# Optimization experiments

Measured on AMD Instinct MI355X. Metric: run time of the kernel, lower is better.

## Reference

```python
import jax, jax.numpy as jnp
import numpy as np

NSITES = 262144
ZP1 = 13  # coordination number Z=12, plus the self row


def setup_inputs() -> dict:
    key = jax.random.key(0)
    k1, k2, k3, k4 = jax.random.split(key, 4)
    In = jax.random.normal(k1, (4, 8, NSITES), dtype=jnp.float32)
    NNsites = jax.random.randint(k2, (ZP1, NSITES), 0, NSITES, dtype=jnp.int32)
    Weights = jax.random.normal(k3, (8, 8, 16), dtype=jnp.float32)  # (K, C_out, 2*C_in)
    bias = jax.random.normal(k4, (8, 8), dtype=jnp.float32)         # (K, C_out)
    return {"In": In, "NNsites": NNsites, "Weights": Weights, "bias": bias}


def reference(In, NNsites, Weights, bias):
    # Original math per neighbor z:
    #   total = concat([In, In[:,:,NN[1+z]]], axis=1)            # (B, 2C_in, N)
    #   o[b,n,k,co] = sum_i W[k,co,i]*total[b,i,n] + bias[k,co]
    #   o summed over channels k, then softplus, accumulated over z.
    # Sum over k commutes with the linear map, so use effective weights.
    C_in = In.shape[1]
    Weff = Weights.sum(axis=0)          # (C_out, 2*C_in)
    beff = bias.sum(axis=0)             # (C_out,)
    Ws, Wn = Weff[:, :C_in], Weff[:, C_in:]
    # self contribution, identical for every z
    self_part = jnp.einsum('oi,bin->bon', Ws, In)          # (B, C_out, N)
    # gather all Z neighbor shells at once: (B, C_in, Z, N)
    neigh = In[:, :, NNsites[1:]]
    neigh_out = jnp.einsum('oi,bizn->bozn', Wn, neigh)     # (B, C_out, Z, N)
    pre = self_part[:, :, None, :] + neigh_out + beff[None, :, None, None]
    return jax.nn.softplus(pre).sum(axis=2)                # (B, C_out, N)
```

## Files before the change

### kernel.cpp

```cpp
#include <hip/hip_runtime.h>
#include <hip/hip_fp16.h>

#define NSITES 262144

struct alignas(16) H8 { __half2 h[4]; };
typedef __attribute__((ext_vector_type(2))) float floatx2;
typedef __attribute__((ext_vector_type(4))) unsigned int uintx4;


__global__ __launch_bounds__(256) void prep_kernel(
    const float* __restrict__ In,
    const float* __restrict__ Weights,
    const float* __restrict__ bias,
    uint2* __restrict__ G8,
    H8*    __restrict__ Sp)
{
    __shared__ float ws[8][8], wn[8][8], be[8];
    int t = threadIdx.x;
    if (t < 64) {
        int o = t >> 3, k = t & 7;
        float s0 = 0.f, s1 = 0.f;
        #pragma unroll
        for (int s = 0; s < 8; ++s) {
            s0 += Weights[s*128 + o*16 + k];
            s1 += Weights[s*128 + o*16 + 8 + k];
        }
        ws[o][k] = s0; wn[o][k] = s1;
    } else if (t < 72) {
        int o = t - 64;
        float s = 0.f;
        #pragma unroll
        for (int q = 0; q < 8; ++q) s += bias[q*8 + o];
        be[o] = s;
    }
    __syncthreads();

    int b    = t & 3;
    int sl   = t >> 2;
    int site = blockIdx.x * 64 + sl;

    float x[8];
    #pragma unroll
    for (int i = 0; i < 8; ++i)
        x[i] = In[(b*8 + i) * NSITES + site];

    float g[8], s[8];
    #pragma unroll
    for (int o = 0; o < 8; ++o) {
        float a0 = 0.f, a1 = be[o];
        #pragma unroll
        for (int i = 0; i < 8; ++i) {
            a0 = fmaf(wn[o][i], x[i], a0);
            a1 = fmaf(ws[o][i], x[i], a1);
        }
        g[o] = a0; s[o] = a1;
    }

    unsigned int w0 = 0, w1 = 0;
    w0 = __builtin_amdgcn_cvt_pk_fp8_f32(g[0], g[1], w0, false);
    w0 = __builtin_amdgcn_cvt_pk_fp8_f32(g[2], g[3], w0, true);
    w1 = __builtin_amdgcn_cvt_pk_fp8_f32(g[4], g[5], w1, false);
    w1 = __builtin_amdgcn_cvt_pk_fp8_f32(g[6], g[7], w1, true);
    G8[site*4 + b] = make_uint2(w0, w1);

    H8 sv;
    #pragma unroll
    for (int p = 0; p < 4; ++p) sv.h[p] = __floats2half2_rn(s[2*p], s[2*p+1]);
    Sp[site*4 + b] = sv;
}

__global__ __launch_bounds__(256) void gather_kernel(
    const H8*    __restrict__ Sp,
    const uint2* __restrict__ G8,
    const int*   __restrict__ NN,
    float*       __restrict__ out)
{
    int t    = threadIdx.x;
    int q    = t & 3;
    int sl   = t >> 2;
    int base = blockIdx.x * 64;
    int n    = base + sl;

    int m[12];
    #pragma unroll
    for (int z = 0; z < 12; ++z)
        m[z] = __builtin_nontemporal_load(&NN[(z + 1) * NSITES + n]);

    uint2 gw[12];
    #pragma unroll
    for (int z = 0; z < 12; ++z)
        gw[z] = G8[m[z] * 4 + q];

    uintx4 spw = __builtin_nontemporal_load((const uintx4*)Sp + (n*4 + q));
    float sp[8];
    #pragma unroll
    for (int p = 0; p < 4; ++p) {
        unsigned int w = spw[p];
        __half2 h; __builtin_memcpy(&h, &w, 4);
        float2 f = __half22float2(h);
        sp[2*p] = f.x; sp[2*p+1] = f.y;
    }

    const float NLOG2E = -1.44269504f;
    float acc[8], prod[8];
    #pragma unroll
    for (int k = 0; k < 8; ++k) { acc[k] = 0.f; prod[k] = 1.f; }

    #pragma unroll
    for (int z = 0; z < 12; ++z) {
        float g[8];
        floatx2 p;
        p = __builtin_amdgcn_cvt_pk_f32_fp8(gw[z].x, false); g[0]=p[0]; g[1]=p[1];
        p = __builtin_amdgcn_cvt_pk_f32_fp8(gw[z].x, true ); g[2]=p[0]; g[3]=p[1];
        p = __builtin_amdgcn_cvt_pk_f32_fp8(gw[z].y, false); g[4]=p[0]; g[5]=p[1];
        p = __builtin_amdgcn_cvt_pk_f32_fp8(gw[z].y, true ); g[6]=p[0]; g[7]=p[1];
        #pragma unroll
        for (int k = 0; k < 8; ++k) {
            float x  = sp[k] + g[k];
            float ax = fabsf(x);
            acc[k] += fmaxf(x, 0.f);
            float e = __builtin_amdgcn_exp2f(ax * NLOG2E);
            prod[k] = fmaf(prod[k], e, prod[k]);
        }
    }

    #pragma unroll
    for (int k = 0; k < 8; ++k) {
        float r = acc[k] + 0.69314718f * __builtin_amdgcn_logf(prod[k]);
        __builtin_nontemporal_store(r, &out[(q*8 + k) * NSITES + n]);
    }
}

extern "C" void kernel_launch(void* const* d_in, const int* in_sizes, int n_in,
                              void* d_out, int out_size, void* d_ws, size_t ws_size,
                              hipStream_t stream) {
    const float* In      = (const float*)d_in[0];
    const int*   NN      = (const int*)  d_in[1];
    const float* Weights = (const float*)d_in[2];
    const float* bias    = (const float*)d_in[3];
    float* out = (float*)d_out;

    uint2* G8 = (uint2*)d_ws;
    H8*    Sp = (H8*)((char*)d_ws + (size_t)NSITES * 32);

    prep_kernel<<<NSITES / 64, 256, 0, stream>>>(In, Weights, bias, G8, Sp);
    gather_kernel<<<NSITES / 64, 256, 0, stream>>>(Sp, G8, NN, out);
}
```

Baseline: 139.5 us.

## Split gather into two batch-half passes to shrink random-access working set

The prep kernel now writes the fp8 neighbor table and fp16 self table as two separate half-batch arrays. The gather runs twice, once per batch pair, so each pass randomly gathers from a 4 MB table instead of 8 MB, which should fit caches better. Each thread handles one batch instead of using four lanes per site, and neighbor loads are moved inside the z loop. The cost is that NN indices are read twice and there is an extra kernel launch.

```diff
diff --git a/kernel.cpp b/kernel.cpp
--- a/kernel.cpp
+++ b/kernel.cpp
@@ -12,8 +12,8 @@
     const float* __restrict__ In,
     const float* __restrict__ Weights,
     const float* __restrict__ bias,
-    uint2* __restrict__ G8,
-    H8*    __restrict__ Sp)
+    uint2* __restrict__ Ga, uint2* __restrict__ Gb,
+    H8*    __restrict__ Spa, H8* __restrict__ Spb)
 {
     __shared__ float ws[8][8], wn[8][8], be[8];
     int t = threadIdx.x;
@@ -61,24 +61,28 @@
     w0 = __builtin_amdgcn_cvt_pk_fp8_f32(g[2], g[3], w0, true);
     w1 = __builtin_amdgcn_cvt_pk_fp8_f32(g[4], g[5], w1, false);
     w1 = __builtin_amdgcn_cvt_pk_fp8_f32(g[6], g[7], w1, true);
-    G8[site*4 + b] = make_uint2(w0, w1);
+
+    uint2* gd = (b < 2) ? Ga : Gb;
+    gd[site*2 + (b & 1)] = make_uint2(w0, w1);
 
     H8 sv;
     #pragma unroll
     for (int p = 0; p < 4; ++p) sv.h[p] = __floats2half2_rn(s[2*p], s[2*p+1]);
-    Sp[site*4 + b] = sv;
+    H8* sd = (b < 2) ? Spa : Spb;
+    sd[site*2 + (b & 1)] = sv;
 }
 
 __global__ __launch_bounds__(256) void gather_kernel(
-    const H8*    __restrict__ Sp,
-    const uint2* __restrict__ G8,
+    const H8*    __restrict__ Sp2,
+    const uint2* __restrict__ G2,
     const int*   __restrict__ NN,
-    float*       __restrict__ out)
+    float*       __restrict__ out,
+    int bofs)
 {
     int t    = threadIdx.x;
-    int q    = t & 3;
-    int sl   = t >> 2;
-    int base = blockIdx.x * 64;
+    int q2   = t & 1;
+    int sl   = t >> 1;
+    int base = blockIdx.x * 128;
     int n    = base + sl;
 
     int m[12];
@@ -86,17 +90,12 @@
     for (int z = 0; z < 12; ++z)
         m[z] = __builtin_nontemporal_load(&NN[(z + 1) * NSITES + n]);
 
-    uint2 gw[12];
-    #pragma unroll
-    for (int z = 0; z < 12; ++z)
-        gw[z] = G8[m[z] * 4 + q];
-
-    uintx4 spw = __builtin_nontemporal_load((const uintx4*)Sp + (n*4 + q));
+    uintx4 spw = __builtin_nontemporal_load((const uintx4*)Sp2 + (n*2 + q2));
     float sp[8];
     #pragma unroll
     for (int p = 0; p < 4; ++p) {
-        unsigned int w = spw[p];
-        __half2 h; __builtin_memcpy(&h, &w, 4);
+        unsigned int wd = spw[p];
+        __half2 h; __builtin_memcpy(&h, &wd, 4);
         float2 f = __half22float2(h);
         sp[2*p] = f.x; sp[2*p+1] = f.y;
     }
@@ -108,12 +107,13 @@
 
     #pragma unroll
     for (int z = 0; z < 12; ++z) {
+        uint2 gw = G2[m[z]*2 + q2];
         float g[8];
         floatx2 p;
-        p = __builtin_amdgcn_cvt_pk_f32_fp8(gw[z].x, false); g[0]=p[0]; g[1]=p[1];
-        p = __builtin_amdgcn_cvt_pk_f32_fp8(gw[z].x, true ); g[2]=p[0]; g[3]=p[1];
-        p = __builtin_amdgcn_cvt_pk_f32_fp8(gw[z].y, false); g[4]=p[0]; g[5]=p[1];
-        p = __builtin_amdgcn_cvt_pk_f32_fp8(gw[z].y, true ); g[6]=p[0]; g[7]=p[1];
+        p = __builtin_amdgcn_cvt_pk_f32_fp8(gw.x, false); g[0]=p[0]; g[1]=p[1];
+        p = __builtin_amdgcn_cvt_pk_f32_fp8(gw.x, true ); g[2]=p[0]; g[3]=p[1];
+        p = __builtin_amdgcn_cvt_pk_f32_fp8(gw.y, false); g[4]=p[0]; g[5]=p[1];
+        p = __builtin_amdgcn_cvt_pk_f32_fp8(gw.y, true ); g[6]=p[0]; g[7]=p[1];
         #pragma unroll
         for (int k = 0; k < 8; ++k) {
             float x  = sp[k] + g[k];
@@ -124,10 +124,11 @@
         }
     }
 
+    int j8 = (bofs + q2) * 8;
     #pragma unroll
     for (int k = 0; k < 8; ++k) {
         float r = acc[k] + 0.69314718f * __builtin_amdgcn_logf(prod[k]);
-        __builtin_nontemporal_store(r, &out[(q*8 + k) * NSITES + n]);
+        __builtin_nontemporal_store(r, &out[(j8 + k) * NSITES + n]);
     }
 }
 
@@ -140,9 +141,13 @@
     const float* bias    = (const float*)d_in[3];
     float* out = (float*)d_out;
 
-    uint2* G8 = (uint2*)d_ws;
-    H8*    Sp = (H8*)((char*)d_ws + (size_t)NSITES * 32);
+    char* w = (char*)d_ws;
+    uint2* Ga  = (uint2*)(w);
+    uint2* Gb  = (uint2*)(w + (size_t)NSITES * 16);
+    H8*    Spa = (H8*)   (w + (size_t)NSITES * 32);
+    H8*    Spb = (H8*)   (w + (size_t)NSITES * 64);
 
-    prep_kernel<<<NSITES / 64, 256, 0, stream>>>(In, Weights, bias, G8, Sp);
-    gather_kernel<<<NSITES / 64, 256, 0, stream>>>(Sp, G8, NN, out);
+    prep_kernel<<<NSITES / 64, 256, 0, stream>>>(In, Weights, bias, Ga, Gb, Spa, Spb);
+    gather_kernel<<<NSITES / 128, 256, 0, stream>>>(Spa, Ga, NN, out, 0);
+    gather_kernel<<<NSITES / 128, 256, 0, stream>>>(Spb, Gb, NN, out, 2);
 }
```

Result: slower. 149.6 us (+7.3%).

## Software-pipeline gather kernel across four site groups per thread

Applied to the files above, without the earlier changes.

The gather kernel now launches 1024 blocks, and each thread handles four sites strided by 65536. Index, neighbor and self-row loads are issued through inline assembly with manual vmcnt waits, so the loads for the next site group overlap the softplus compute and stores of the current one. The aim is to hide the latency of dependent gathers without relying only on occupancy. In exchange, register pressure rises from the double-buffered arrays, there are fewer resident waves per CU, and the hand-written wait counts make the code fragile.

```diff
diff --git a/kernel.cpp b/kernel.cpp
--- a/kernel.cpp
+++ b/kernel.cpp
@@ -2,9 +2,12 @@
 #include <hip/hip_fp16.h>
 
 #define NSITES 262144
+#define NB 1024
+#define USTRIDE 65536
 
 struct alignas(16) H8 { __half2 h[4]; };
 typedef __attribute__((ext_vector_type(2))) float floatx2;
+typedef __attribute__((ext_vector_type(2))) unsigned int uintx2;
 typedef __attribute__((ext_vector_type(4))) unsigned int uintx4;
 
 
@@ -75,60 +78,106 @@
     const int*   __restrict__ NN,
     float*       __restrict__ out)
 {
-    int t    = threadIdx.x;
-    int q    = t & 3;
-    int sl   = t >> 2;
-    int base = blockIdx.x * 64;
-    int n    = base + sl;
+    int t  = threadIdx.x;
+    int q  = t & 3;
+    int sl = t >> 2;
+    int n0 = blockIdx.x * 64 + sl;
 
-    int m[12];
-    #pragma unroll
-    for (int z = 0; z < 12; ++z)
-        m[z] = __builtin_nontemporal_load(&NN[(z + 1) * NSITES + n]);
+    int    m[2][12];
+    uintx2 gw[2][12];
+    uintx4 spw[2];
 
-    uint2 gw[12];
-    #pragma unroll
-    for (int z = 0; z < 12; ++z)
-        gw[z] = G8[m[z] * 4 + q];
+#define NN_ISSUE(BUF, U) do {                                                  \
+    _Pragma("unroll")                                                          \
+    for (int z_ = 0; z_ < 12; ++z_) {                                          \
+        const int* p_ = NN + (z_ + 1) * NSITES + (n0 + (U) * USTRIDE);         \
+        asm volatile("global_load_dword %0, %1, off nt"                        \
+                     : "=v"(m[BUF][z_]) : "v"(p_));                            \
+    } } while (0)
 
-    uintx4 spw = __builtin_nontemporal_load((const uintx4*)Sp + (n*4 + q));
-    float sp[8];
-    #pragma unroll
-    for (int p = 0; p < 4; ++p) {
-        unsigned int w = spw[p];
-        __half2 h; __builtin_memcpy(&h, &w, 4);
-        float2 f = __half22float2(h);
-        sp[2*p] = f.x; sp[2*p+1] = f.y;
-    }
+#define G_ISSUE(BUF) do {                                                      \
+    _Pragma("unroll")                                                          \
+    for (int z_ = 0; z_ < 12; ++z_) {                                          \
+        const uint2* p_ = G8 + (m[BUF][z_] * 4 + q);                           \
+        asm volatile("global_load_dwordx2 %0, %1, off"                         \
+                     : "=v"(gw[BUF][z_]) : "v"(p_));                           \
+    } } while (0)
 
-    const float NLOG2E = -1.44269504f;
-    float acc[8], prod[8];
-    #pragma unroll
-    for (int k = 0; k < 8; ++k) { acc[k] = 0.f; prod[k] = 1.f; }
+#define SP_ISSUE(BUF, U) do {                                                  \
+    const uintx4* p_ = (const uintx4*)Sp + ((n0 + (U) * USTRIDE) * 4 + q);     \
+    asm volatile("global_load_dwordx4 %0, %1, off nt"                          \
+                 : "=v"(spw[BUF]) : "v"(p_));                                  \
+    } while (0)
 
-    #pragma unroll
-    for (int z = 0; z < 12; ++z) {
-        float g[8];
-        floatx2 p;
-        p = __builtin_amdgcn_cvt_pk_f32_fp8(gw[z].x, false); g[0]=p[0]; g[1]=p[1];
-        p = __builtin_amdgcn_cvt_pk_f32_fp8(gw[z].x, true ); g[2]=p[0]; g[3]=p[1];
-        p = __builtin_amdgcn_cvt_pk_f32_fp8(gw[z].y, false); g[4]=p[0]; g[5]=p[1];
-        p = __builtin_amdgcn_cvt_pk_f32_fp8(gw[z].y, true ); g[6]=p[0]; g[7]=p[1];
-        #pragma unroll
-        for (int k = 0; k < 8; ++k) {
-            float x  = sp[k] + g[k];
-            float ax = fabsf(x);
-            acc[k] += fmaxf(x, 0.f);
-            float e = __builtin_amdgcn_exp2f(ax * NLOG2E);
-            prod[k] = fmaf(prod[k], e, prod[k]);
-        }
-    }
+#define COMPUTE_STORE(U, BUF) do {                                             \
+    float sp_[8];                                                              \
+    _Pragma("unroll")                                                          \
+    for (int p_ = 0; p_ < 4; ++p_) {                                           \
+        unsigned int wd_ = spw[BUF][p_];                                       \
+        __half2 h_; __builtin_memcpy(&h_, &wd_, 4);                            \
+        float2 f_ = __half22float2(h_);                                        \
+        sp_[2*p_] = f_.x; sp_[2*p_+1] = f_.y;                                  \
+    }                                                                          \
+    float acc_[8], prod_[8];                                                   \
+    _Pragma("unroll")                                                          \
+    for (int k_ = 0; k_ < 8; ++k_) { acc_[k_] = 0.f; prod_[k_] = 1.f; }        \
+    _Pragma("unroll")                                                          \
+    for (int z_ = 0; z_ < 12; ++z_) {                                          \
+        unsigned int gx_ = gw[BUF][z_][0];                                     \
+        unsigned int gy_ = gw[BUF][z_][1];                                     \
+        float g_[8]; floatx2 pp_;                                              \
+        pp_ = __builtin_amdgcn_cvt_pk_f32_fp8(gx_, false); g_[0]=pp_[0]; g_[1]=pp_[1]; \
+        pp_ = __builtin_amdgcn_cvt_pk_f32_fp8(gx_, true ); g_[2]=pp_[0]; g_[3]=pp_[1]; \
+        pp_ = __builtin_amdgcn_cvt_pk_f32_fp8(gy_, false); g_[4]=pp_[0]; g_[5]=pp_[1]; \
+        pp_ = __builtin_amdgcn_cvt_pk_f32_fp8(gy_, true ); g_[6]=pp_[0]; g_[7]=pp_[1]; \
+        _Pragma("unroll")                                                      \
+        for (int k_ = 0; k_ < 8; ++k_) {                                       \
+            float x_  = sp_[k_] + g_[k_];                                      \
+            float ax_ = fabsf(x_);                                             \
+            acc_[k_] += fmaxf(x_, 0.f);                                        \
+            float e_ = __builtin_amdgcn_exp2f(ax_ * -1.44269504f);             \
+            prod_[k_] = fmaf(prod_[k_], e_, prod_[k_]);                        \
+        }                                                                      \
+    }                                                                          \
+    int n_ = n0 + (U) * USTRIDE;                                               \
+    _Pragma("unroll")                                                          \
+    for (int k_ = 0; k_ < 8; ++k_) {                                           \
+        float r_ = acc_[k_] + 0.69314718f * __builtin_amdgcn_logf(prod_[k_]);  \
+        float* op_ = out + (q*8 + k_) * NSITES + n_;                           \
+        asm volatile("global_store_dword %0, %1, off nt" :: "v"(op_), "v"(r_)); \
+    } } while (0)
 
-    #pragma unroll
-    for (int k = 0; k < 8; ++k) {
-        float r = acc[k] + 0.69314718f * __builtin_amdgcn_logf(prod[k]);
-        __builtin_nontemporal_store(r, &out[(q*8 + k) * NSITES + n]);
-    }
+#define WAITV(N) do {                                                          \
+    asm volatile("s_waitcnt vmcnt(" #N ")" ::: "memory");                      \
+    __builtin_amdgcn_sched_barrier(0); } while (0)
+
+    NN_ISSUE(0, 0);
+    NN_ISSUE(1, 1);
+    WAITV(12);
+    G_ISSUE(0); SP_ISSUE(0, 0);
+
+    WAITV(0);
+    G_ISSUE(1); SP_ISSUE(1, 1);
+    NN_ISSUE(0, 2);
+    COMPUTE_STORE(0, 0);
+
+    WAITV(8);
+    G_ISSUE(0); SP_ISSUE(0, 2);
+    NN_ISSUE(1, 3);
+    COMPUTE_STORE(1, 1);
+
+    WAITV(8);
+    G_ISSUE(1); SP_ISSUE(1, 3);
+    COMPUTE_STORE(2, 0);
+
+    WAITV(8);
+    COMPUTE_STORE(3, 1);
+
+#undef NN_ISSUE
+#undef G_ISSUE
+#undef SP_ISSUE
+#undef COMPUTE_STORE
+#undef WAITV
 }
 
 extern "C" void kernel_launch(void* const* d_in, const int* in_sizes, int n_in,
@@ -144,5 +193,5 @@
     H8*    Sp = (H8*)((char*)d_ws + (size_t)NSITES * 32);
 
     prep_kernel<<<NSITES / 64, 256, 0, stream>>>(In, Weights, bias, G8, Sp);
-    gather_kernel<<<NSITES / 64, 256, 0, stream>>>(Sp, G8, NN, out);
+    gather_kernel<<<NB, 256, 0, stream>>>(Sp, G8, NN, out);
 }
```

New measurement: 138.6 us. About the same (-0.6%).

## Split gather tables per batch and map blocks to batch-site pairs

Applied to the files above, without the earlier changes.

The precomputed neighbor table and self table move from site-major interleaved batches (site*4+b) to batch-major planes (b*NSITES+site). The gather kernel now gives each thread one site and one batch, and a block index swizzle spreads the four batch planes over neighboring blocks. Each random gather fetches 8 bytes from one per-batch 2 MB plane instead of a 32-byte shared line. This aims at cache locality per plane (and, likely, XCD placement), but every site's neighbor indices are now loaded four times, once per batch block, instead of once.

```diff
diff --git a/kernel.cpp b/kernel.cpp
--- a/kernel.cpp
+++ b/kernel.cpp
@@ -12,8 +12,8 @@
     const float* __restrict__ In,
     const float* __restrict__ Weights,
     const float* __restrict__ bias,
-    uint2* __restrict__ G8,
-    H8*    __restrict__ Sp)
+    uint2* __restrict__ Gs,
+    H8*    __restrict__ Ss)
 {
     __shared__ float ws[8][8], wn[8][8], be[8];
     int t = threadIdx.x;
@@ -35,16 +35,16 @@
     }
     __syncthreads();
 
-    int b    = t & 3;
-    int sl   = t >> 2;
-    int site = blockIdx.x * 64 + sl;
+    int b    = t >> 6;
+    int lane = t & 63;
+    int site = blockIdx.x * 64 + lane;
 
     float x[8];
     #pragma unroll
     for (int i = 0; i < 8; ++i)
         x[i] = In[(b*8 + i) * NSITES + site];
 
-    float g[8], s[8];
+    float g[8], sv[8];
     #pragma unroll
     for (int o = 0; o < 8; ++o) {
         float a0 = 0.f, a1 = be[o];
@@ -53,7 +53,7 @@
             a0 = fmaf(wn[o][i], x[i], a0);
             a1 = fmaf(ws[o][i], x[i], a1);
         }
-        g[o] = a0; s[o] = a1;
+        g[o] = a0; sv[o] = a1;
     }
 
     unsigned int w0 = 0, w1 = 0;
@@ -61,42 +61,40 @@
     w0 = __builtin_amdgcn_cvt_pk_fp8_f32(g[2], g[3], w0, true);
     w1 = __builtin_amdgcn_cvt_pk_fp8_f32(g[4], g[5], w1, false);
     w1 = __builtin_amdgcn_cvt_pk_fp8_f32(g[6], g[7], w1, true);
-    G8[site*4 + b] = make_uint2(w0, w1);
+    Gs[b * NSITES + site] = make_uint2(w0, w1);
 
-    H8 sv;
+    H8 hv;
     #pragma unroll
-    for (int p = 0; p < 4; ++p) sv.h[p] = __floats2half2_rn(s[2*p], s[2*p+1]);
-    Sp[site*4 + b] = sv;
+    for (int p = 0; p < 4; ++p) hv.h[p] = __floats2half2_rn(sv[2*p], sv[2*p+1]);
+    Ss[b * NSITES + site] = hv;
 }
 
 __global__ __launch_bounds__(256) void gather_kernel(
-    const H8*    __restrict__ Sp,
-    const uint2* __restrict__ G8,
+    const H8*    __restrict__ Ss,
+    const uint2* __restrict__ Gs,
     const int*   __restrict__ NN,
     float*       __restrict__ out)
 {
-    int t    = threadIdx.x;
-    int q    = t & 3;
-    int sl   = t >> 2;
-    int base = blockIdx.x * 64;
-    int n    = base + sl;
+    int bid = blockIdx.x;
+    int g   = (bid & 7) >> 1;
+    int c   = ((bid >> 3) << 1) | (bid & 1);
+    int t   = threadIdx.x;
+    int n   = c * 256 + t;
+
+    const uint2* Gb = Gs + (size_t)g * NSITES;
 
     int m[12];
     #pragma unroll
     for (int z = 0; z < 12; ++z)
         m[z] = __builtin_nontemporal_load(&NN[(z + 1) * NSITES + n]);
 
-    uint2 gw[12];
-    #pragma unroll
-    for (int z = 0; z < 12; ++z)
-        gw[z] = G8[m[z] * 4 + q];
-
-    uintx4 spw = __builtin_nontemporal_load((const uintx4*)Sp + (n*4 + q));
+    uintx4 spw = __builtin_nontemporal_load(
+        (const uintx4*)(Ss + (size_t)g * NSITES) + n);
     float sp[8];
     #pragma unroll
     for (int p = 0; p < 4; ++p) {
-        unsigned int w = spw[p];
-        __half2 h; __builtin_memcpy(&h, &w, 4);
+        unsigned int wd = spw[p];
+        __half2 h; __builtin_memcpy(&h, &wd, 4);
         float2 f = __half22float2(h);
         sp[2*p] = f.x; sp[2*p+1] = f.y;
     }
@@ -108,15 +106,16 @@
 
     #pragma unroll
     for (int z = 0; z < 12; ++z) {
-        float g[8];
+        uint2 gw = Gb[m[z]];
+        float gv[8];
         floatx2 p;
-        p = __builtin_amdgcn_cvt_pk_f32_fp8(gw[z].x, false); g[0]=p[0]; g[1]=p[1];
-        p = __builtin_amdgcn_cvt_pk_f32_fp8(gw[z].x, true ); g[2]=p[0]; g[3]=p[1];
-        p = __builtin_amdgcn_cvt_pk_f32_fp8(gw[z].y, false); g[4]=p[0]; g[5]=p[1];
-        p = __builtin_amdgcn_cvt_pk_f32_fp8(gw[z].y, true ); g[6]=p[0]; g[7]=p[1];
+        p = __builtin_amdgcn_cvt_pk_f32_fp8(gw.x, false); gv[0]=p[0]; gv[1]=p[1];
+        p = __builtin_amdgcn_cvt_pk_f32_fp8(gw.x, true ); gv[2]=p[0]; gv[3]=p[1];
+        p = __builtin_amdgcn_cvt_pk_f32_fp8(gw.y, false); gv[4]=p[0]; gv[5]=p[1];
+        p = __builtin_amdgcn_cvt_pk_f32_fp8(gw.y, true ); gv[6]=p[0]; gv[7]=p[1];
         #pragma unroll
         for (int k = 0; k < 8; ++k) {
-            float x  = sp[k] + g[k];
+            float x  = sp[k] + gv[k];
             float ax = fabsf(x);
             acc[k] += fmaxf(x, 0.f);
             float e = __builtin_amdgcn_exp2f(ax * NLOG2E);
@@ -127,7 +126,7 @@
     #pragma unroll
     for (int k = 0; k < 8; ++k) {
         float r = acc[k] + 0.69314718f * __builtin_amdgcn_logf(prod[k]);
-        __builtin_nontemporal_store(r, &out[(q*8 + k) * NSITES + n]);
+        __builtin_nontemporal_store(r, &out[(g*8 + k) * NSITES + n]);
     }
 }
 
@@ -140,9 +139,9 @@
     const float* bias    = (const float*)d_in[3];
     float* out = (float*)d_out;
 
-    uint2* G8 = (uint2*)d_ws;
-    H8*    Sp = (H8*)((char*)d_ws + (size_t)NSITES * 32);
+    uint2* Gs = (uint2*)d_ws;
+    H8*    Ss = (H8*)((char*)d_ws + (size_t)NSITES * 32);
 
-    prep_kernel<<<NSITES / 64, 256, 0, stream>>>(In, Weights, bias, G8, Sp);
-    gather_kernel<<<NSITES / 64, 256, 0, stream>>>(Sp, G8, NN, out);
+    prep_kernel<<<NSITES / 64, 256, 0, stream>>>(In, Weights, bias, Gs, Ss);
+    gather_kernel<<<NSITES / 64, 256, 0, stream>>>(Ss, Gs, NN, out);
 }
```

Result: slower. 164.0 us (+17.6%).
